# Kernel tuning notes

Hardware: AMD Instinct MI355X
Metric: run time of the kernel (lower is better)

The kernel has to match this reference:

```python
import jax, jax.numpy as jnp
import numpy as np

N = 262144          # total nodes
D = 256             # feature dim
D_OUT = 128
NUM_SEGMENTS = 4096 # number of graphs/sets


def setup_inputs() -> dict:
    key = jax.random.key(0)
    ks = jax.random.split(key, 8)
    sc = 1.0 / np.sqrt(D)
    x = jax.random.normal(ks[0], (N, D), dtype=jnp.float32)
    index = jnp.sort(jax.random.randint(ks[1], (N,), 0, NUM_SEGMENTS)).astype(jnp.int32)
    W1 = jax.random.normal(ks[2], (D, D), dtype=jnp.float32) * sc
    b1 = jnp.zeros((D,), dtype=jnp.float32)
    W2 = jax.random.normal(ks[3], (D, D), dtype=jnp.float32) * sc
    b2 = jnp.zeros((D,), dtype=jnp.float32)
    W3 = jax.random.normal(ks[4], (D, D), dtype=jnp.float32) * sc
    b3 = jnp.zeros((D,), dtype=jnp.float32)
    W4 = jax.random.normal(ks[5], (D, D_OUT), dtype=jnp.float32) * sc
    b4 = jnp.zeros((D_OUT,), dtype=jnp.float32)
    return {"x": x, "index": index, "W1": W1, "b1": b1, "W2": W2, "b2": b2,
            "W3": W3, "b3": b3, "W4": W4, "b4": b4}


def reference(x, index, W1, b1, W2, b2, W3, b3, W4, b4):
    # score_net: 2-layer SiLU MLP, per node -> scores s [N, D]
    s = jax.nn.silu(x @ W1 + b1) @ W2 + b2
    # scatter_softmax over nodes grouped by segment index (dim=0)
    m = jax.ops.segment_max(s, index, num_segments=NUM_SEGMENTS)  # [B, D]
    e = jnp.exp(s - jax.lax.stop_gradient(m)[index])              # [N, D]
    denom = jax.ops.segment_sum(e, index, num_segments=NUM_SEGMENTS)  # [B, D]
    attn = e / denom[index]                                       # [N, D]
    # weighted segment sum: sum_splits(s * x, splits)
    sx = jax.ops.segment_sum(attn * x, index, num_segments=NUM_SEGMENTS)  # [B, D]
    # readout_net: 2-layer SiLU MLP per segment
    out = jax.nn.silu(sx @ W3 + b3) @ W4 + b4                     # [B, D_OUT]
    return out
```

## Files before the change

kernel.cpp:

```cpp
#include <hip/hip_runtime.h>

typedef _Float16 half8 __attribute__((ext_vector_type(8)));
typedef float f32x4 __attribute__((ext_vector_type(4)));

#define LDS_AS __attribute__((address_space(3)))
#define GLB_AS __attribute__((address_space(1)))

__device__ __forceinline__ void load_lds16(const void* g, void* l) {
    __builtin_amdgcn_global_load_lds((const GLB_AS unsigned int*)g,
                                     (LDS_AS unsigned int*)l, 16, 0, 0);
}

#define GRIDF 256
#define TPB   32

__global__ void prep_weights(const float* __restrict__ W1, const float* __restrict__ W2,
                             const float* __restrict__ W3, const float* __restrict__ W4,
                             _Float16* __restrict__ W1t, _Float16* __restrict__ W2t,
                             _Float16* __restrict__ W3t, _Float16* __restrict__ W4t) {
    int e = blockIdx.x * 256 + threadIdx.x;
    if (e < 196608) {
        int sel = e >> 16, r = e & 65535;
        const float* src = sel == 0 ? W1 : (sel == 1 ? W2 : W3);
        _Float16* dst = sel == 0 ? W1t : (sel == 1 ? W2t : W3t);
        int n = r >> 8, k = r & 255;
        dst[n * 256 + k] = (_Float16)src[k * 256 + n];
    } else {
        int r = e - 196608;
        int n = r >> 8, k = r & 255;
        W4t[n * 256 + k] = (_Float16)W4[k * 128 + n];
    }
}

__global__ __launch_bounds__(512, 2)
void fused(const float* __restrict__ x, const _Float16* __restrict__ W1t,
           const float* __restrict__ b1, const _Float16* __restrict__ W2t,
           const float* __restrict__ b2, const int* __restrict__ index,
           float* __restrict__ gnum, float* __restrict__ gden)
{
    __shared__ __align__(16) float Abuf[2][32 * 256];
    __shared__ __align__(16) _Float16 Hh[32 * 256];
    __shared__ __align__(16) float etile[32 * 257];
    __shared__ int sl[32];

    const int tid = threadIdx.x;
    const int w = tid >> 6, lane = tid & 63;
    const int q = lane >> 4, l15 = lane & 15;

    half8 Bf1[2][8], Bf2[2][8];
#pragma unroll
    for (int j = 0; j < 2; ++j)
#pragma unroll
        for (int kc = 0; kc < 8; ++kc) {
            Bf1[j][kc] = *(const half8*)(W1t + (size_t)(w * 32 + j * 16 + l15) * 256 + kc * 32 + q * 8);
            Bf2[j][kc] = *(const half8*)(W2t + (size_t)(w * 32 + j * 16 + l15) * 256 + kc * 32 + q * 8);
        }
    float b1v[2], b2v[2];
#pragma unroll
    for (int j = 0; j < 2; ++j) {
        b1v[j] = b1[w * 32 + j * 16 + l15];
        b2v[j] = b2[w * 32 + j * 16 + l15];
    }

    const int t0 = blockIdx.x * TPB;

    auto stage = [&](int b, int t) {
        const float* src = x + (size_t)t * 32 * 256;
#pragma unroll
        for (int p = 0; p < 4; ++p) {
            int c = p * 512 + tid;
            int r = c >> 6, pc = c & 63;
            int lc = pc ^ (r & 7);
            load_lds16(src + (size_t)r * 256 + lc * 4, &Abuf[b][c * 4]);
        }
    };

    float aN = 0.f, aD = 0.f;
    int curseg = -1;

    int cur = 0;
    stage(0, t0);
#pragma unroll 1
    for (int ti = 0; ti < TPB; ++ti) {
        const int t = t0 + ti;
        __syncthreads();
        if (tid < 32) sl[tid] = index[t * 32 + tid];
        if (ti + 1 < TPB) stage(cur ^ 1, t + 1);

        const float* Ab = Abuf[cur];

        f32x4 acc[2][2];
#pragma unroll
        for (int i = 0; i < 2; ++i)
#pragma unroll
            for (int j = 0; j < 2; ++j) acc[i][j] = (f32x4){0.f, 0.f, 0.f, 0.f};

#pragma unroll
        for (int kc = 0; kc < 8; ++kc) {
            half8 af[2];
#pragma unroll
            for (int i = 0; i < 2; ++i) {
                int row = i * 16 + l15;
                int s = row & 7;
                f32x4 lo = *(const f32x4*)(Ab + row * 256 + (((kc * 8 + q * 2) ^ s) * 4));
                f32x4 hi = *(const f32x4*)(Ab + row * 256 + (((kc * 8 + q * 2 + 1) ^ s) * 4));
#pragma unroll
                for (int c = 0; c < 4; ++c) { af[i][c] = (_Float16)lo[c]; af[i][4 + c] = (_Float16)hi[c]; }
            }
#pragma unroll
            for (int i = 0; i < 2; ++i)
#pragma unroll
                for (int j = 0; j < 2; ++j)
                    acc[i][j] = __builtin_amdgcn_mfma_f32_16x16x32_f16(af[i], Bf1[j][kc], acc[i][j], 0, 0, 0);
        }

#pragma unroll
        for (int i = 0; i < 2; ++i)
#pragma unroll
            for (int j = 0; j < 2; ++j)
#pragma unroll
                for (int r = 0; r < 4; ++r) {
                    float v = acc[i][j][r] + b1v[j];
                    float sv = v / (1.f + __expf(-v));
                    int row = i * 16 + q * 4 + r;
                    int col = w * 32 + j * 16 + l15;
                    int unit = (col >> 3) ^ (row & 7);
                    Hh[row * 256 + unit * 8 + (col & 7)] = (_Float16)sv;
                }
        __syncthreads();

        f32x4 acc2[2][2];
#pragma unroll
        for (int i = 0; i < 2; ++i)
#pragma unroll
            for (int j = 0; j < 2; ++j) acc2[i][j] = (f32x4){0.f, 0.f, 0.f, 0.f};

#pragma unroll
        for (int kc = 0; kc < 8; ++kc) {
            half8 af[2];
#pragma unroll
            for (int i = 0; i < 2; ++i) {
                int row = i * 16 + l15;
                af[i] = *(const half8*)(Hh + row * 256 + (((kc * 4 + q) ^ (row & 7)) * 8));
            }
#pragma unroll
            for (int i = 0; i < 2; ++i)
#pragma unroll
                for (int j = 0; j < 2; ++j)
                    acc2[i][j] = __builtin_amdgcn_mfma_f32_16x16x32_f16(af[i], Bf2[j][kc], acc2[i][j], 0, 0, 0);
        }

#pragma unroll
        for (int i = 0; i < 2; ++i)
#pragma unroll
            for (int j = 0; j < 2; ++j)
#pragma unroll
                for (int r = 0; r < 4; ++r)
                    etile[(i * 16 + q * 4 + r) * 257 + w * 32 + j * 16 + l15] =
                        __expf(acc2[i][j][r] + b2v[j]);
        __syncthreads();

        if (tid < 256) {
            const int col = tid;
#pragma unroll 1
            for (int hb = 0; hb < 2; ++hb) {
                float xv[16];
#pragma unroll
                for (int r = 0; r < 16; ++r) {
                    int rr = hb * 16 + r;
                    xv[r] = Ab[rr * 256 + ((((col >> 2) ^ (rr & 7)) << 2) | (col & 3))];
                }
#pragma unroll
                for (int r = 0; r < 16; ++r) {
                    int rr = hb * 16 + r;
                    int sg = sl[rr];
                    if (sg != curseg) {
                        if (curseg >= 0) {
                            atomicAdd(&gnum[(size_t)curseg * 256 + col], aN);
                            atomicAdd(&gden[(size_t)curseg * 256 + col], aD);
                        }
                        aN = 0.f; aD = 0.f; curseg = sg;
                    }
                    float e = etile[rr * 257 + col];
                    aN += e * xv[r];
                    aD += e;
                }
            }
        }
        cur ^= 1;
    }
    if (tid < 256 && curseg >= 0) {
        atomicAdd(&gnum[(size_t)curseg * 256 + tid], aN);
        atomicAdd(&gden[(size_t)curseg * 256 + tid], aD);
    }
}

__global__ void normalize_sx(const float* __restrict__ num, const float* __restrict__ den,
                             _Float16* __restrict__ sx) {
    int i = blockIdx.x * 256 + threadIdx.x;
    float d = den[i];
    sx[i] = (_Float16)((d > 0.f) ? num[i] / d : 0.f);
}

__global__ __launch_bounds__(256, 2)
void readout1(const _Float16* __restrict__ sx, const _Float16* __restrict__ W3t,
              const float* __restrict__ b3, _Float16* __restrict__ h2)
{
    __shared__ __align__(16) _Float16 Ah[64 * 256];
    const int tid = threadIdx.x;
    const int w = tid >> 6, lane = tid & 63;
    const int q = lane >> 4, l15 = lane & 15;
    const int row0 = blockIdx.x * 64;

    half8 Bf[4][8];
#pragma unroll
    for (int j = 0; j < 4; ++j)
#pragma unroll
        for (int kc = 0; kc < 8; ++kc)
            Bf[j][kc] = *(const half8*)(W3t + (size_t)(w * 64 + j * 16 + l15) * 256 + kc * 32 + q * 8);
    float bv[4];
#pragma unroll
    for (int j = 0; j < 4; ++j) bv[j] = b3[w * 64 + j * 16 + l15];

#pragma unroll
    for (int p = 0; p < 8; ++p) {
        int c = p * 256 + tid;
        int r = c >> 5, pc = c & 31;
        int lc = pc ^ (r & 7);
        load_lds16(sx + (size_t)(row0 + r) * 256 + lc * 8, &Ah[c * 8]);
    }
    __syncthreads();

    f32x4 acc[4][4];
#pragma unroll
    for (int i = 0; i < 4; ++i)
#pragma unroll
        for (int j = 0; j < 4; ++j) acc[i][j] = (f32x4){0.f, 0.f, 0.f, 0.f};

#pragma unroll
    for (int kc = 0; kc < 8; ++kc) {
        half8 af[4];
#pragma unroll
        for (int i = 0; i < 4; ++i) {
            int row = i * 16 + l15;
            af[i] = *(const half8*)(Ah + row * 256 + (((kc * 4 + q) ^ (row & 7)) * 8));
        }
#pragma unroll
        for (int i = 0; i < 4; ++i)
#pragma unroll
            for (int j = 0; j < 4; ++j)
                acc[i][j] = __builtin_amdgcn_mfma_f32_16x16x32_f16(af[i], Bf[j][kc], acc[i][j], 0, 0, 0);
    }
#pragma unroll
    for (int i = 0; i < 4; ++i)
#pragma unroll
        for (int j = 0; j < 4; ++j)
#pragma unroll
            for (int r = 0; r < 4; ++r) {
                float v = acc[i][j][r] + bv[j];
                float sv = v / (1.f + __expf(-v));
                h2[(size_t)(row0 + i * 16 + q * 4 + r) * 256 + w * 64 + j * 16 + l15] = (_Float16)sv;
            }
}

__global__ __launch_bounds__(256, 2)
void readout2(const _Float16* __restrict__ h2, const _Float16* __restrict__ W4t,
              const float* __restrict__ b4, float* __restrict__ out)
{
    __shared__ __align__(16) _Float16 Ah[64 * 256];
    const int tid = threadIdx.x;
    const int w = tid >> 6, lane = tid & 63;
    const int q = lane >> 4, l15 = lane & 15;
    const int row0 = blockIdx.x * 64;

    half8 Bf[2][8];
#pragma unroll
    for (int j = 0; j < 2; ++j)
#pragma unroll
        for (int kc = 0; kc < 8; ++kc)
            Bf[j][kc] = *(const half8*)(W4t + (size_t)(w * 32 + j * 16 + l15) * 256 + kc * 32 + q * 8);
    float bv[2];
#pragma unroll
    for (int j = 0; j < 2; ++j) bv[j] = b4[w * 32 + j * 16 + l15];

#pragma unroll
    for (int p = 0; p < 8; ++p) {
        int c = p * 256 + tid;
        int r = c >> 5, pc = c & 31;
        int lc = pc ^ (r & 7);
        load_lds16(h2 + (size_t)(row0 + r) * 256 + lc * 8, &Ah[c * 8]);
    }
    __syncthreads();

    f32x4 acc[4][2];
#pragma unroll
    for (int i = 0; i < 4; ++i)
#pragma unroll
        for (int j = 0; j < 2; ++j) acc[i][j] = (f32x4){0.f, 0.f, 0.f, 0.f};

#pragma unroll
    for (int kc = 0; kc < 8; ++kc) {
        half8 af[4];
#pragma unroll
        for (int i = 0; i < 4; ++i) {
            int row = i * 16 + l15;
            af[i] = *(const half8*)(Ah + row * 256 + (((kc * 4 + q) ^ (row & 7)) * 8));
        }
#pragma unroll
        for (int i = 0; i < 4; ++i)
#pragma unroll
            for (int j = 0; j < 2; ++j)
                acc[i][j] = __builtin_amdgcn_mfma_f32_16x16x32_f16(af[i], Bf[j][kc], acc[i][j], 0, 0, 0);
    }
#pragma unroll
    for (int i = 0; i < 4; ++i)
#pragma unroll
        for (int j = 0; j < 2; ++j)
#pragma unroll
            for (int r = 0; r < 4; ++r)
                out[(size_t)(row0 + i * 16 + q * 4 + r) * 128 + w * 32 + j * 16 + l15] =
                    acc[i][j][r] + bv[j];
}

extern "C" void kernel_launch(void* const* d_in, const int* in_sizes, int n_in,
                              void* d_out, int out_size, void* d_ws, size_t ws_size,
                              hipStream_t stream) {
    const float* x   = (const float*)d_in[0];
    const int*   idx = (const int*)d_in[1];
    const float* W1  = (const float*)d_in[2];
    const float* b1  = (const float*)d_in[3];
    const float* W2  = (const float*)d_in[4];
    const float* b2  = (const float*)d_in[5];
    const float* W3  = (const float*)d_in[6];
    const float* b3  = (const float*)d_in[7];
    const float* W4  = (const float*)d_in[8];
    const float* b4  = (const float*)d_in[9];
    char* ws = (char*)d_ws;

    float*    gnum = (float*)ws;
    float*    gden = (float*)(ws + 4194304);
    _Float16* sx   = (_Float16*)(ws + 8388608);
    _Float16* h2   = (_Float16*)(ws + 10485760);
    _Float16* W1t  = (_Float16*)(ws + 12582912);
    _Float16* W2t  = (_Float16*)(ws + 12713984);
    _Float16* W3t  = (_Float16*)(ws + 12845056);
    _Float16* W4t  = (_Float16*)(ws + 12976128);

    prep_weights<<<896, 256, 0, stream>>>(W1, W2, W3, W4, W1t, W2t, W3t, W4t);
    hipMemsetAsync(ws, 0, 8388608, stream);

    fused<<<GRIDF, 512, 0, stream>>>(x, W1t, b1, W2t, b2, idx, gnum, gden);

    normalize_sx<<<4096, 256, 0, stream>>>(gnum, gden, sx);
    readout1<<<64, 256, 0, stream>>>(sx, W3t, b3, h2);
    readout2<<<64, 256, 0, stream>>>(h2, W4t, b4, (float*)d_out);
}
```

Measured before the change: 476.4 us.

## Single-buffer x tile to raise occupancy, read x and index from global in epilogue

Drops the double-buffered x tile and the segment-id LDS array, shrinking LDS so four 512-thread blocks can fit per CU instead of two, and doubles the grid while halving tiles per block. The next tile's prefetch now starts after the first GEMM, overlapping only with the second GEMM and the epilogue. The epilogue rereads x and the segment index from global memory (likely cache hits), and the etile padding is replaced by an XOR swizzle. SiLU uses a hardware reciprocal instead of a division. The costs are less load/compute overlap and more global traffic in the epilogue, and the higher occupancy target may cause register spills given the large per-thread weight fragments.

```diff
diff --git a/kernel.cpp b/kernel.cpp
--- a/kernel.cpp
+++ b/kernel.cpp
@@ -11,8 +11,8 @@
                                      (LDS_AS unsigned int*)l, 16, 0, 0);
 }
 
-#define GRIDF 256
-#define TPB   32
+#define GRIDF 512
+#define TPB   16
 
 __global__ void prep_weights(const float* __restrict__ W1, const float* __restrict__ W2,
                              const float* __restrict__ W3, const float* __restrict__ W4,
@@ -32,16 +32,15 @@
     }
 }
 
-__global__ __launch_bounds__(512, 2)
+__global__ __launch_bounds__(512, 4)
 void fused(const float* __restrict__ x, const _Float16* __restrict__ W1t,
            const float* __restrict__ b1, const _Float16* __restrict__ W2t,
            const float* __restrict__ b2, const int* __restrict__ index,
            float* __restrict__ gnum, float* __restrict__ gden)
 {
-    __shared__ __align__(16) float Abuf[2][32 * 256];
+    __shared__ __align__(16) float Abuf[32 * 256];
     __shared__ __align__(16) _Float16 Hh[32 * 256];
-    __shared__ __align__(16) float etile[32 * 257];
-    __shared__ int sl[32];
+    __shared__ __align__(16) float etile[32 * 256];
 
     const int tid = threadIdx.x;
     const int w = tid >> 6, lane = tid & 63;
@@ -64,30 +63,25 @@
 
     const int t0 = blockIdx.x * TPB;
 
-    auto stage = [&](int b, int t) {
+    auto stage = [&](int t) {
         const float* src = x + (size_t)t * 32 * 256;
 #pragma unroll
         for (int p = 0; p < 4; ++p) {
             int c = p * 512 + tid;
             int r = c >> 6, pc = c & 63;
             int lc = pc ^ (r & 7);
-            load_lds16(src + (size_t)r * 256 + lc * 4, &Abuf[b][c * 4]);
+            load_lds16(src + (size_t)r * 256 + lc * 4, &Abuf[c * 4]);
         }
     };
 
     float aN = 0.f, aD = 0.f;
     int curseg = -1;
 
-    int cur = 0;
-    stage(0, t0);
+    stage(t0);
 #pragma unroll 1
     for (int ti = 0; ti < TPB; ++ti) {
         const int t = t0 + ti;
         __syncthreads();
-        if (tid < 32) sl[tid] = index[t * 32 + tid];
-        if (ti + 1 < TPB) stage(cur ^ 1, t + 1);
-
-        const float* Ab = Abuf[cur];
 
         f32x4 acc[2][2];
 #pragma unroll
@@ -102,8 +96,8 @@
             for (int i = 0; i < 2; ++i) {
                 int row = i * 16 + l15;
                 int s = row & 7;
-                f32x4 lo = *(const f32x4*)(Ab + row * 256 + (((kc * 8 + q * 2) ^ s) * 4));
-                f32x4 hi = *(const f32x4*)(Ab + row * 256 + (((kc * 8 + q * 2 + 1) ^ s) * 4));
+                f32x4 lo = *(const f32x4*)(Abuf + row * 256 + (((kc * 8 + q * 2) ^ s) * 4));
+                f32x4 hi = *(const f32x4*)(Abuf + row * 256 + (((kc * 8 + q * 2 + 1) ^ s) * 4));
 #pragma unroll
                 for (int c = 0; c < 4; ++c) { af[i][c] = (_Float16)lo[c]; af[i][4 + c] = (_Float16)hi[c]; }
             }
@@ -121,7 +115,7 @@
 #pragma unroll
                 for (int r = 0; r < 4; ++r) {
                     float v = acc[i][j][r] + b1v[j];
-                    float sv = v / (1.f + __expf(-v));
+                    float sv = v * __builtin_amdgcn_rcpf(1.f + __expf(-v));
                     int row = i * 16 + q * 4 + r;
                     int col = w * 32 + j * 16 + l15;
                     int unit = (col >> 3) ^ (row & 7);
@@ -129,6 +123,8 @@
                 }
         __syncthreads();
 
+        if (ti + 1 < TPB) stage(t + 1);
+
         f32x4 acc2[2][2];
 #pragma unroll
         for (int i = 0; i < 2; ++i)
@@ -155,25 +151,27 @@
 #pragma unroll
             for (int j = 0; j < 2; ++j)
 #pragma unroll
-                for (int r = 0; r < 4; ++r)
-                    etile[(i * 16 + q * 4 + r) * 257 + w * 32 + j * 16 + l15] =
+                for (int r = 0; r < 4; ++r) {
+                    int row = i * 16 + q * 4 + r;
+                    int col = w * 32 + j * 16 + l15;
+                    etile[row * 256 + (col ^ ((row & 7) << 2))] =
                         __expf(acc2[i][j][r] + b2v[j]);
+                }
         __syncthreads();
 
         if (tid < 256) {
             const int col = tid;
+            const float* gx = x + (size_t)t * 32 * 256 + col;
 #pragma unroll 1
             for (int hb = 0; hb < 2; ++hb) {
                 float xv[16];
 #pragma unroll
+                for (int r = 0; r < 16; ++r)
+                    xv[r] = gx[(size_t)(hb * 16 + r) * 256];
+#pragma unroll
                 for (int r = 0; r < 16; ++r) {
                     int rr = hb * 16 + r;
-                    xv[r] = Ab[rr * 256 + ((((col >> 2) ^ (rr & 7)) << 2) | (col & 3))];
-                }
-#pragma unroll
-                for (int r = 0; r < 16; ++r) {
-                    int rr = hb * 16 + r;
-                    int sg = sl[rr];
+                    int sg = index[t * 32 + rr];
                     if (sg != curseg) {
                         if (curseg >= 0) {
                             atomicAdd(&gnum[(size_t)curseg * 256 + col], aN);
@@ -181,13 +179,12 @@
                         }
                         aN = 0.f; aD = 0.f; curseg = sg;
                     }
-                    float e = etile[rr * 257 + col];
+                    float e = etile[rr * 256 + (col ^ ((rr & 7) << 2))];
                     aN += e * xv[r];
                     aD += e;
                 }
             }
         }
-        cur ^= 1;
     }
     if (tid < 256 && curseg >= 0) {
         atomicAdd(&gnum[(size_t)curseg * 256 + tid], aN);
```

Result: slower. 794.6 us (+66.8%).

## Stage x as fp16 in LDS via registers and precompute e*x in fp16 pairs

Applied to the files above, without the earlier changes.

The x tile now goes through registers and is converted to fp16 before it is written to LDS, replacing the async global-to-LDS copy of fp32. This halves the LDS footprint and removes the per-MFMA conversion. The epilogue computes e and e*x together and stores them as a swizzled fp16 pair, so the segment-reduction loop reads one packed value per row. SiLU now uses a reciprocal instruction instead of a division. The trade-off is register-staged prefetch instead of async LDS loads, and fp16 rounding of e and e*x before accumulation, which risks overflow or precision loss because e is not max-subtracted.

```diff
diff --git a/kernel.cpp b/kernel.cpp
--- a/kernel.cpp
+++ b/kernel.cpp
@@ -1,6 +1,8 @@
 #include <hip/hip_runtime.h>
 
 typedef _Float16 half8 __attribute__((ext_vector_type(8)));
+typedef _Float16 half4 __attribute__((ext_vector_type(4)));
+typedef _Float16 half2v __attribute__((ext_vector_type(2)));
 typedef float f32x4 __attribute__((ext_vector_type(4)));
 
 #define LDS_AS __attribute__((address_space(3)))
@@ -38,9 +40,9 @@
            const float* __restrict__ b2, const int* __restrict__ index,
            float* __restrict__ gnum, float* __restrict__ gden)
 {
-    __shared__ __align__(16) float Abuf[2][32 * 256];
+    __shared__ __align__(16) _Float16 Abuf[2][32 * 256];
     __shared__ __align__(16) _Float16 Hh[32 * 256];
-    __shared__ __align__(16) float etile[32 * 257];
+    __shared__ __align__(16) half2v ep[32 * 256];
     __shared__ int sl[32];
 
     const int tid = threadIdx.x;
@@ -64,30 +66,36 @@
 
     const int t0 = blockIdx.x * TPB;
 
-    auto stage = [&](int b, int t) {
-        const float* src = x + (size_t)t * 32 * 256;
+    f32x4 sreg[4];
+    auto stage_load = [&](int t) {
+        const f32x4* src = (const f32x4*)(x + (size_t)t * 8192);
+#pragma unroll
+        for (int p = 0; p < 4; ++p) sreg[p] = src[p * 512 + tid];
+    };
+    auto stage_write = [&](int b) {
 #pragma unroll
         for (int p = 0; p < 4; ++p) {
             int c = p * 512 + tid;
-            int r = c >> 6, pc = c & 63;
-            int lc = pc ^ (r & 7);
-            load_lds16(src + (size_t)r * 256 + lc * 4, &Abuf[b][c * 4]);
+            int row = c >> 6, k0 = (c & 63) * 4;
+            int unit = (k0 >> 3) ^ (row & 7);
+            half4 h = { (_Float16)sreg[p][0], (_Float16)sreg[p][1],
+                        (_Float16)sreg[p][2], (_Float16)sreg[p][3] };
+            *(half4*)&Abuf[b][row * 256 + unit * 8 + (k0 & 7)] = h;
         }
     };
 
     float aN = 0.f, aD = 0.f;
     int curseg = -1;
 
+    stage_load(t0);
+    stage_write(0);
     int cur = 0;
-    stage(0, t0);
 #pragma unroll 1
     for (int ti = 0; ti < TPB; ++ti) {
         const int t = t0 + ti;
         __syncthreads();
         if (tid < 32) sl[tid] = index[t * 32 + tid];
-        if (ti + 1 < TPB) stage(cur ^ 1, t + 1);
-
-        const float* Ab = Abuf[cur];
+        if (ti + 1 < TPB) stage_load(t + 1);
 
         f32x4 acc[2][2];
 #pragma unroll
@@ -101,11 +109,7 @@
 #pragma unroll
             for (int i = 0; i < 2; ++i) {
                 int row = i * 16 + l15;
-                int s = row & 7;
-                f32x4 lo = *(const f32x4*)(Ab + row * 256 + (((kc * 8 + q * 2) ^ s) * 4));
-                f32x4 hi = *(const f32x4*)(Ab + row * 256 + (((kc * 8 + q * 2 + 1) ^ s) * 4));
-#pragma unroll
-                for (int c = 0; c < 4; ++c) { af[i][c] = (_Float16)lo[c]; af[i][4 + c] = (_Float16)hi[c]; }
+                af[i] = *(const half8*)(&Abuf[cur][row * 256 + (((kc * 4 + q) ^ (row & 7)) * 8)]);
             }
 #pragma unroll
             for (int i = 0; i < 2; ++i)
@@ -121,7 +125,7 @@
 #pragma unroll
                 for (int r = 0; r < 4; ++r) {
                     float v = acc[i][j][r] + b1v[j];
-                    float sv = v / (1.f + __expf(-v));
+                    float sv = v * __builtin_amdgcn_rcpf(1.f + __expf(-v));
                     int row = i * 16 + q * 4 + r;
                     int col = w * 32 + j * 16 + l15;
                     int unit = (col >> 3) ^ (row & 7);
@@ -155,36 +159,33 @@
 #pragma unroll
             for (int j = 0; j < 2; ++j)
 #pragma unroll
-                for (int r = 0; r < 4; ++r)
-                    etile[(i * 16 + q * 4 + r) * 257 + w * 32 + j * 16 + l15] =
-                        __expf(acc2[i][j][r] + b2v[j]);
+                for (int r = 0; r < 4; ++r) {
+                    int row = i * 16 + q * 4 + r;
+                    int col = w * 32 + j * 16 + l15;
+                    float ev = __expf(acc2[i][j][r] + b2v[j]);
+                    float xv = (float)Abuf[cur][row * 256 + ((((col >> 3) ^ (row & 7)) << 3) | (col & 7))];
+                    ep[row * 256 + (col ^ ((row & 7) << 2))] =
+                        (half2v){ (_Float16)ev, (_Float16)(ev * xv) };
+                }
         __syncthreads();
+
+        if (ti + 1 < TPB) stage_write(cur ^ 1);
 
         if (tid < 256) {
             const int col = tid;
-#pragma unroll 1
-            for (int hb = 0; hb < 2; ++hb) {
-                float xv[16];
-#pragma unroll
-                for (int r = 0; r < 16; ++r) {
-                    int rr = hb * 16 + r;
-                    xv[r] = Ab[rr * 256 + ((((col >> 2) ^ (rr & 7)) << 2) | (col & 3))];
+#pragma unroll
+            for (int rr = 0; rr < 32; ++rr) {
+                int sg = sl[rr];
+                if (sg != curseg) {
+                    if (curseg >= 0) {
+                        atomicAdd(&gnum[(size_t)curseg * 256 + col], aN);
+                        atomicAdd(&gden[(size_t)curseg * 256 + col], aD);
+                    }
+                    aN = 0.f; aD = 0.f; curseg = sg;
                 }
-#pragma unroll
-                for (int r = 0; r < 16; ++r) {
-                    int rr = hb * 16 + r;
-                    int sg = sl[rr];
-                    if (sg != curseg) {
-                        if (curseg >= 0) {
-                            atomicAdd(&gnum[(size_t)curseg * 256 + col], aN);
-                            atomicAdd(&gden[(size_t)curseg * 256 + col], aD);
-                        }
-                        aN = 0.f; aD = 0.f; curseg = sg;
-                    }
-                    float e = etile[rr * 257 + col];
-                    aN += e * xv[r];
-                    aD += e;
-                }
+                half2v hv = ep[rr * 256 + (col ^ ((rr & 7) << 2))];
+                aD += (float)hv[0];
+                aN += (float)hv[1];
             }
         }
         cur ^= 1;
```

Result: slower. 514.8 us (+8.1%).
